# Optimization experiments

Measured on AMD Instinct MI355X. Metric: run time of the kernel, lower is better.

The kernel has to match this reference:

```python
import jax, jax.numpy as jnp
import numpy as np

V = 50304   # vocab
P = 1024    # max positions
D = 768     # model dim
H = 12      # heads
HD = D // H # head dim (64)
L = 12      # depth
M = 4       # mlp ratio
B = 2
S = 1024
LN_EPS_BLOCK = 1e-6
LN_EPS_FINAL = 1e-5


def setup_inputs() -> dict:
    key = jax.random.key(0)
    ks = jax.random.split(key, 16)
    def n(k, shape, s=0.02):
        return (jax.random.normal(k, shape) * s).astype(jnp.float32)
    inp = {
        'input_ids': jax.random.randint(ks[0], (B, S), 0, V, dtype=jnp.int64) if jax.config.jax_enable_x64 else jax.random.randint(ks[0], (B, S), 0, V).astype(jnp.int32),
        'attention_mask': jnp.ones((B, S), jnp.float32),
        'wte': n(ks[1], (V, D)),
        'wpe': n(ks[2], (P, D)),
        'ln1_g': jnp.ones((L, D), jnp.float32),
        'ln1_b': jnp.zeros((L, D), jnp.float32),
        'qkv_w': n(ks[3], (L, D, 3 * D)),
        'qkv_b': jnp.zeros((L, 3 * D), jnp.float32),
        'proj_w': n(ks[4], (L, D, D)),
        'proj_b': jnp.zeros((L, D), jnp.float32),
        'ln2_g': jnp.ones((L, D), jnp.float32),
        'ln2_b': jnp.zeros((L, D), jnp.float32),
        'fc1_w': n(ks[5], (L, D, M * D)),
        'fc1_b': jnp.zeros((L, M * D), jnp.float32),
        'fc2_w': n(ks[6], (L, M * D, D)),
        'fc2_b': jnp.zeros((L, D), jnp.float32),
        'lnf_g': jnp.ones((D,), jnp.float32),
        'lnf_b': jnp.zeros((D,), jnp.float32),
        'head_b': jnp.zeros((V,), jnp.float32),
    }
    return inp


def _ln(x, g, b, eps):
    mu = jnp.mean(x, -1, keepdims=True)
    var = jnp.mean(jnp.square(x - mu), -1, keepdims=True)
    return (x - mu) * jax.lax.rsqrt(var + eps) * g + b


def _block(x, mask_add, p):
    (g1, b1, wqkv, bqkv, wp, bp, g2, b2, w1, b1m, w2, b2m) = p
    h = _ln(x, g1, b1, LN_EPS_BLOCK)
    qkv = h @ wqkv + bqkv                                  # [B,S,3D]
    qkv = qkv.reshape(x.shape[0], x.shape[1], H, 3 * HD).transpose(0, 2, 1, 3)
    q, k, v = jnp.split(qkv, 3, axis=-1)                   # each [B,H,S,hd]
    scores = jnp.einsum('bhqd,bhkd->bhqk', q, k) / np.float32(np.sqrt(HD))
    causal = jnp.tril(jnp.ones((x.shape[1], x.shape[1]), bool))
    scores = jnp.where(causal, scores, jnp.float32(-10000.0))
    scores = scores + mask_add
    probs = jax.nn.softmax(scores, axis=-1)
    o = jnp.einsum('bhqk,bhkd->bhqd', probs, v)
    o = o.transpose(0, 2, 1, 3).reshape(x.shape[0], x.shape[1], D)
    x = x + (o @ wp + bp)
    h = _ln(x, g2, b2, LN_EPS_BLOCK)
    h = jax.nn.gelu(h @ w1 + b1m, approximate=False)
    x = x + (h @ w2 + b2m)
    return x


def reference(input_ids, attention_mask, wte, wpe, ln1_g, ln1_b, qkv_w, qkv_b,
              proj_w, proj_b, ln2_g, ln2_b, fc1_w, fc1_b, fc2_w, fc2_b,
              lnf_g, lnf_b, head_b):
    seq = input_ids.shape[1]
    mask_add = (1.0 - attention_mask)[:, None, None, :] * jnp.float32(-10000.0)
    x = wte[input_ids] + wpe[jnp.arange(seq)][None]         # [B,S,D]
    layer_params = (ln1_g, ln1_b, qkv_w, qkv_b, proj_w, proj_b,
                    ln2_g, ln2_b, fc1_w, fc1_b, fc2_w, fc2_b)
    def step(h, p):
        return _block(h, mask_add, p), None
    x, _ = jax.lax.scan(step, x, layer_params)
    x = _ln(x, lnf_g, lnf_b, LN_EPS_FINAL)
    logits = x @ wte.T + head_b                             # tied LM head
    return logits
```

## Files before the change

kernel.cpp:

```cpp
#include <hip/hip_runtime.h>
#include <hip/hip_bf16.h>

typedef unsigned short u16;
typedef short bf16x8 __attribute__((ext_vector_type(8)));
typedef float floatx4 __attribute__((ext_vector_type(4)));
typedef u16 u16x4 __attribute__((ext_vector_type(4)));

#define DEV __device__ __forceinline__

DEV u16 f2bf(float f) {
    unsigned u = __builtin_bit_cast(unsigned, f);
    u += 0x7fffu + ((u >> 16) & 1u);
    return (u16)(u >> 16);
}
DEV float bf2f(u16 h) {
    unsigned u = ((unsigned)h) << 16;
    return __builtin_bit_cast(float, u);
}

static constexpr int Dm   = 768;
static constexpr int Hn   = 12;
static constexpr int HDn  = 64;
static constexpr int Ln   = 12;
static constexpr int Vn   = 50304;
static constexpr int Sn   = 1024;
static constexpr int Bn   = 2;
static constexpr int Tn   = Bn * Sn;
static constexpr int DMLP = 4 * Dm;

#define GLOAD_LDS16(gptr, lptr)                                                        \
    __builtin_amdgcn_global_load_lds((const __attribute__((address_space(1))) void*)(gptr), \
                                     (__attribute__((address_space(3))) void*)(lptr), 16, 0, 0)

__global__ __launch_bounds__(256) void k_cvt(const float* __restrict__ s,
                                             u16* __restrict__ d, int n4) {
    int i = blockIdx.x * 256 + threadIdx.x;
    if (i >= n4) return;
    const float4 v = *(const float4*)(s + (size_t)i * 4);
    u16x4 o;
    o[0] = f2bf(v.x); o[1] = f2bf(v.y); o[2] = f2bf(v.z); o[3] = f2bf(v.w);
    *(u16x4*)(d + (size_t)i * 4) = o;
}

__global__ __launch_bounds__(256) void k_tr(const float* __restrict__ src,
                                            u16* __restrict__ dst, int R, int C) {
    __shared__ float tile[32][33];
    const int l = blockIdx.z;
    src += (size_t)l * R * C;
    dst += (size_t)l * R * C;
    const int c0 = blockIdx.x * 32, r0 = blockIdx.y * 32;
    const int tx = threadIdx.x, ty = threadIdx.y;
#pragma unroll
    for (int i = 0; i < 4; i++)
        tile[ty + i * 8][tx] = src[(size_t)(r0 + ty + i * 8) * C + c0 + tx];
    __syncthreads();
#pragma unroll
    for (int i = 0; i < 4; i++)
        dst[(size_t)(c0 + ty + i * 8) * R + r0 + tx] = f2bf(tile[tx][ty + i * 8]);
}

__global__ __launch_bounds__(256) void k_embed(const int* __restrict__ ids,
                                               const float* __restrict__ wte,
                                               const float* __restrict__ wpe,
                                               float* __restrict__ x) {
    int idx = blockIdx.x * 256 + threadIdx.x;
    int t = idx / Dm, d = idx - t * Dm;
    int s = t & (Sn - 1);
    x[idx] = wte[(size_t)ids[t] * Dm + d] + wpe[(size_t)s * Dm + d];
}

__global__ __launch_bounds__(256) void k_ln(const float* __restrict__ x,
                                            const float* __restrict__ g,
                                            const float* __restrict__ bvec,
                                            u16* __restrict__ out, float eps) {
    const int row = blockIdx.x, tid = threadIdx.x;
    const float* xr = x + (size_t)row * Dm;
    float v0 = xr[tid], v1 = xr[tid + 256], v2 = xr[tid + 512];
    float s = v0 + v1 + v2;
    float q = v0 * v0 + v1 * v1 + v2 * v2;
#pragma unroll
    for (int off = 1; off < 64; off <<= 1) {
        s += __shfl_xor(s, off, 64);
        q += __shfl_xor(q, off, 64);
    }
    __shared__ float red[8];
    const int wid = tid >> 6;
    if ((tid & 63) == 0) { red[wid] = s; red[4 + wid] = q; }
    __syncthreads();
    s = red[0] + red[1] + red[2] + red[3];
    q = red[4] + red[5] + red[6] + red[7];
    const float mu  = s * (1.0f / Dm);
    const float var = q * (1.0f / Dm) - mu * mu;
    const float rs  = rsqrtf(var + eps);
    u16* orow = out + (size_t)row * Dm;
    orow[tid]       = f2bf((v0 - mu) * rs * g[tid]       + bvec[tid]);
    orow[tid + 256] = f2bf((v1 - mu) * rs * g[tid + 256] + bvec[tid + 256]);
    orow[tid + 512] = f2bf((v2 - mu) * rs * g[tid + 512] + bvec[tid + 512]);
}

template <int MODE>
__global__ __launch_bounds__(256) void k_gemm(const u16* __restrict__ A,
                                              const u16* __restrict__ W,
                                              const float* __restrict__ bias,
                                              float* __restrict__ outF,
                                              u16* __restrict__ outB,
                                              u16* __restrict__ outQ,
                                              u16* __restrict__ outK,
                                              u16* __restrict__ outV,
                                              int M, int N, int K) {
    __shared__ u16 sA[128 * 64];
    __shared__ u16 sW[128 * 64];
    const int tid = threadIdx.x;
    const int lane = tid & 63, wid = tid >> 6;
    const int lane16 = lane & 15, quad = lane >> 4;
    const int gx = gridDim.x;
    int bid = blockIdx.y * gx + blockIdx.x;
    bid = (bid & 7) * ((gx * gridDim.y) >> 3) + (bid >> 3);
    const int m0 = (bid % gx) * 128, n0 = (bid / gx) * 128;
    const int wm = wid & 1, wn = wid >> 1;

    floatx4 acc[4][4];
#pragma unroll
    for (int i = 0; i < 4; i++)
#pragma unroll
        for (int j = 0; j < 4; j++) acc[i][j] = (floatx4){0.f, 0.f, 0.f, 0.f};

    int kbeg = 0, kend = K;
    if (MODE == 4) {
        const int Kpart = K / (int)gridDim.z;
        kbeg = blockIdx.z * Kpart;
        kend = kbeg + Kpart;
    }

    for (int kb = kbeg; kb < kend; kb += 64) {
#pragma unroll
        for (int it = 0; it < 4; ++it) {
            int p = it * 256 + tid;
            int row = p >> 3;
            int kc = (p & 7) ^ (row & 7);
            GLOAD_LDS16(A + (size_t)(m0 + row) * K + kb + kc * 8, sA + p * 8);
            GLOAD_LDS16(W + (size_t)(n0 + row) * K + kb + kc * 8, sW + p * 8);
        }
        __syncthreads();
#pragma unroll
        for (int ks = 0; ks < 2; ++ks) {
            bf16x8 af[4], wf[4];
#pragma unroll
            for (int i = 0; i < 4; i++) {
                int m = wm * 64 + i * 16 + lane16;
                int ch = (ks * 4 + quad) ^ (m & 7);
                af[i] = *(const bf16x8*)(sA + m * 64 + ch * 8);
            }
#pragma unroll
            for (int j = 0; j < 4; j++) {
                int n = wn * 64 + j * 16 + lane16;
                int ch = (ks * 4 + quad) ^ (n & 7);
                wf[j] = *(const bf16x8*)(sW + n * 64 + ch * 8);
            }
#pragma unroll
            for (int i = 0; i < 4; i++)
#pragma unroll
                for (int j = 0; j < 4; j++)
                    acc[i][j] = __builtin_amdgcn_mfma_f32_16x16x32_bf16(af[i], wf[j], acc[i][j], 0, 0, 0);
        }
        __syncthreads();
    }

#pragma unroll
    for (int i = 0; i < 4; i++) {
        int rowb = m0 + wm * 64 + i * 16 + quad * 4;
#pragma unroll
        for (int j = 0; j < 4; j++) {
            int col = n0 + wn * 64 + j * 16 + lane16;
            float bc = bias[col];
            if (MODE == 3) {
                int h = col / 192, rem = col - h * 192;
                int which = rem >> 6, d = rem & 63;
                u16* dst = (which == 0) ? outQ : (which == 1) ? outK : outV;
                float scale = (which == 0) ? 0.125f : 1.0f;
#pragma unroll
                for (int r = 0; r < 4; r++) {
                    int t = rowb + r;
                    int b = t >> 10, s = t & (Sn - 1);
                    size_t o = ((size_t)(b * Hn + h) * Sn + s) * HDn + d;
                    dst[o] = f2bf((acc[i][j][r] + bc) * scale);
                }
            } else {
#pragma unroll
                for (int r = 0; r < 4; r++) {
                    size_t off = (size_t)(rowb + r) * N + col;
                    if (MODE == 0) {
                        outF[off] = acc[i][j][r] + bc;
                    } else if (MODE == 2) {
                        float v = acc[i][j][r] + bc;
                        float gl = 0.5f * v * (1.0f + erff(v * 0.70710678118654752f));
                        outB[off] = f2bf(gl);
                    } else {
                        float v = acc[i][j][r];
                        if (blockIdx.z == 0) v += bc;
                        atomicAdd(outF + off, v);
                    }
                }
            }
        }
    }
}

__global__ __launch_bounds__(256) void k_attn(const u16* __restrict__ Q,
                                              const u16* __restrict__ Kg,
                                              const u16* __restrict__ Vg,
                                              const float* __restrict__ amask,
                                              u16* __restrict__ out) {
    __shared__ u16 sQ[64 * 72];
    __shared__ u16 sK[64 * 72];
    __shared__ u16 sV[64 * 72];
    __shared__ u16 sP[64 * 72];
    const int tid = threadIdx.x;
    const int lane = tid & 63, wid = tid >> 6;
    const int lane16 = lane & 15, quad = lane >> 4;
    const int blk = blockIdx.x;
    const int qt = blk & 15, bh = blk >> 4;
    const int b = bh / Hn, h = bh - b * Hn;
    const int q0 = qt * 64;
    const u16* Qb = Q + (size_t)bh * Sn * HDn;
    const u16* Kb = Kg + (size_t)bh * Sn * HDn;
    const u16* Vb = Vg + (size_t)bh * Sn * HDn;
    const float* maskb = amask + (size_t)b * Sn;

#pragma unroll
    for (int it = 0; it < 2; ++it) {
        int c = it * 256 + tid;
        int row = c >> 3, kc = c & 7;
        *(bf16x8*)(sQ + row * 72 + kc * 8) = *(const bf16x8*)(Qb + (size_t)(q0 + row) * HDn + kc * 8);
    }

    float mrow[4], lrow[4];
    floatx4 o[4];
#pragma unroll
    for (int r = 0; r < 4; r++) { mrow[r] = -1e30f; lrow[r] = 0.f; }
#pragma unroll
    for (int t = 0; t < 4; t++) o[t] = (floatx4){0.f, 0.f, 0.f, 0.f};

    for (int kt = 0; kt <= qt; ++kt) {
        __syncthreads();
        const int k0 = kt * 64;
#pragma unroll
        for (int it = 0; it < 2; ++it) {
            int c = it * 256 + tid;
            int row = c >> 3, kc = c & 7;
            bf16x8 kv = *(const bf16x8*)(Kb + (size_t)(k0 + row) * HDn + kc * 8);
            *(bf16x8*)(sK + row * 72 + kc * 8) = kv;
            bf16x8 vv = *(const bf16x8*)(Vb + (size_t)(k0 + row) * HDn + kc * 8);
#pragma unroll
            for (int u = 0; u < 8; u++) sV[(kc * 8 + u) * 72 + row] = (u16)vv[u];
        }
        __syncthreads();

        floatx4 s[4];
#pragma unroll
        for (int t = 0; t < 4; t++) s[t] = (floatx4){0.f, 0.f, 0.f, 0.f};
#pragma unroll
        for (int ks = 0; ks < 2; ++ks) {
            bf16x8 aq = *(const bf16x8*)(sQ + (wid * 16 + lane16) * 72 + ks * 32 + quad * 8);
#pragma unroll
            for (int t = 0; t < 4; t++) {
                bf16x8 bk = *(const bf16x8*)(sK + (t * 16 + lane16) * 72 + ks * 32 + quad * 8);
                s[t] = __builtin_amdgcn_mfma_f32_16x16x32_bf16(aq, bk, s[t], 0, 0, 0);
            }
        }

        float madd[4];
#pragma unroll
        for (int t = 0; t < 4; t++)
            madd[t] = (1.0f - maskb[k0 + t * 16 + lane16]) * -10000.0f;
#pragma unroll
        for (int t = 0; t < 4; t++) {
            int kg = k0 + t * 16 + lane16;
#pragma unroll
            for (int r = 0; r < 4; r++) {
                int qg = q0 + wid * 16 + quad * 4 + r;
                float val = s[t][r];
                if (kg > qg) val = -10000.0f;
                s[t][r] = val + madd[t];
            }
        }

        float mnew[4], alpha[4], rsum[4];
#pragma unroll
        for (int r = 0; r < 4; r++) {
            float mx = fmaxf(fmaxf(s[0][r], s[1][r]), fmaxf(s[2][r], s[3][r]));
#pragma unroll
            for (int off = 1; off < 16; off <<= 1) mx = fmaxf(mx, __shfl_xor(mx, off, 64));
            mnew[r] = fmaxf(mrow[r], mx);
            alpha[r] = expf(mrow[r] - mnew[r]);
            rsum[r] = 0.f;
        }
#pragma unroll
        for (int t = 0; t < 4; t++) {
#pragma unroll
            for (int r = 0; r < 4; r++) {
                float p = expf(s[t][r] - mnew[r]);
                rsum[r] += p;
                sP[(wid * 16 + quad * 4 + r) * 72 + t * 16 + lane16] = f2bf(p);
            }
        }
#pragma unroll
        for (int r = 0; r < 4; r++) {
#pragma unroll
            for (int off = 1; off < 16; off <<= 1) rsum[r] += __shfl_xor(rsum[r], off, 64);
            lrow[r] = lrow[r] * alpha[r] + rsum[r];
            mrow[r] = mnew[r];
        }
#pragma unroll
        for (int t = 0; t < 4; t++)
#pragma unroll
            for (int r = 0; r < 4; r++) o[t][r] *= alpha[r];

        __builtin_amdgcn_wave_barrier();

#pragma unroll
        for (int ks = 0; ks < 2; ++ks) {
            bf16x8 ap = *(const bf16x8*)(sP + (wid * 16 + lane16) * 72 + ks * 32 + quad * 8);
#pragma unroll
            for (int t = 0; t < 4; t++) {
                bf16x8 bv = *(const bf16x8*)(sV + (t * 16 + lane16) * 72 + ks * 32 + quad * 8);
                o[t] = __builtin_amdgcn_mfma_f32_16x16x32_bf16(ap, bv, o[t], 0, 0, 0);
            }
        }
    }

#pragma unroll
    for (int t = 0; t < 4; t++) {
#pragma unroll
        for (int r = 0; r < 4; r++) {
            int qg = q0 + wid * 16 + quad * 4 + r;
            float val = o[t][r] / lrow[r];
            out[(size_t)(b * Sn + qg) * Dm + h * HDn + t * 16 + lane16] = f2bf(val);
        }
    }
}

extern "C" void kernel_launch(void* const* d_in, const int* in_sizes, int n_in,
                              void* d_out, int out_size, void* d_ws, size_t ws_size,
                              hipStream_t stream) {
    (void)in_sizes; (void)n_in; (void)out_size; (void)ws_size;

    const int*   ids   = (const int*)  d_in[0];
    const float* amask = (const float*)d_in[1];
    const float* wte   = (const float*)d_in[2];
    const float* wpe   = (const float*)d_in[3];
    const float* ln1g  = (const float*)d_in[4];
    const float* ln1b  = (const float*)d_in[5];
    const float* qkvw  = (const float*)d_in[6];
    const float* qkvb  = (const float*)d_in[7];
    const float* projw = (const float*)d_in[8];
    const float* projb = (const float*)d_in[9];
    const float* ln2g  = (const float*)d_in[10];
    const float* ln2b  = (const float*)d_in[11];
    const float* fc1w  = (const float*)d_in[12];
    const float* fc1b  = (const float*)d_in[13];
    const float* fc2w  = (const float*)d_in[14];
    const float* fc2b  = (const float*)d_in[15];
    const float* lnfg  = (const float*)d_in[16];
    const float* lnfb  = (const float*)d_in[17];
    const float* headb = (const float*)d_in[18];

    char* w = (char*)d_ws;
    u16* wteB = (u16*)w;   w += (size_t)Vn * Dm * 2;
    u16* qkvW = (u16*)w;   w += (size_t)Ln * Dm * 3 * Dm * 2;
    u16* projW = (u16*)w;  w += (size_t)Ln * Dm * Dm * 2;
    u16* fc1W = (u16*)w;   w += (size_t)Ln * Dm * DMLP * 2;
    u16* fc2W = (u16*)w;   w += (size_t)Ln * DMLP * Dm * 2;
    float* x  = (float*)w; w += (size_t)Tn * Dm * 4;
    u16* hbuf = (u16*)w;   w += (size_t)Tn * Dm * 2;
    u16* qb   = (u16*)w;   w += (size_t)Tn * Dm * 2;
    u16* kb   = (u16*)w;   w += (size_t)Tn * Dm * 2;
    u16* vb   = (u16*)w;   w += (size_t)Tn * Dm * 2;
    u16* attn = (u16*)w;   w += (size_t)Tn * Dm * 2;
    u16* mlp  = (u16*)w;   w += (size_t)Tn * DMLP * 2;

    k_cvt<<<(Vn * Dm / 4) / 256, 256, 0, stream>>>(wte, wteB, Vn * Dm / 4);
    dim3 tb(32, 8);
    k_tr<<<dim3(3 * Dm / 32, Dm / 32, Ln), tb, 0, stream>>>(qkvw, qkvW, Dm, 3 * Dm);
    k_tr<<<dim3(Dm / 32, Dm / 32, Ln), tb, 0, stream>>>(projw, projW, Dm, Dm);
    k_tr<<<dim3(DMLP / 32, Dm / 32, Ln), tb, 0, stream>>>(fc1w, fc1W, Dm, DMLP);
    k_tr<<<dim3(Dm / 32, DMLP / 32, Ln), tb, 0, stream>>>(fc2w, fc2W, DMLP, Dm);

    k_embed<<<Tn * Dm / 256, 256, 0, stream>>>(ids, wte, wpe, x);

    for (int l = 0; l < Ln; ++l) {
        k_ln<<<Tn, 256, 0, stream>>>(x, ln1g + l * Dm, ln1b + l * Dm, hbuf, 1e-6f);
        k_gemm<3><<<dim3(Tn / 128, 3 * Dm / 128), 256, 0, stream>>>(
            hbuf, qkvW + (size_t)l * 3 * Dm * Dm, qkvb + l * 3 * Dm,
            nullptr, nullptr, qb, kb, vb, Tn, 3 * Dm, Dm);
        k_attn<<<Bn * Hn * (Sn / 64), 256, 0, stream>>>(qb, kb, vb, amask, attn);
        k_gemm<4><<<dim3(Tn / 128, Dm / 128, 4), 256, 0, stream>>>(
            attn, projW + (size_t)l * Dm * Dm, projb + l * Dm,
            x, nullptr, nullptr, nullptr, nullptr, Tn, Dm, Dm);
        k_ln<<<Tn, 256, 0, stream>>>(x, ln2g + l * Dm, ln2b + l * Dm, hbuf, 1e-6f);
        k_gemm<2><<<dim3(Tn / 128, DMLP / 128), 256, 0, stream>>>(
            hbuf, fc1W + (size_t)l * Dm * DMLP, fc1b + l * DMLP,
            nullptr, mlp, nullptr, nullptr, nullptr, Tn, DMLP, Dm);
        k_gemm<4><<<dim3(Tn / 128, Dm / 128, 4), 256, 0, stream>>>(
            mlp, fc2W + (size_t)l * DMLP * Dm, fc2b + l * Dm,
            x, nullptr, nullptr, nullptr, nullptr, Tn, Dm, DMLP);
    }

    k_ln<<<Tn, 256, 0, stream>>>(x, lnfg, lnfb, hbuf, 1e-5f);
    k_gemm<0><<<dim3(Tn / 128, Vn / 128), 256, 0, stream>>>(
        hbuf, wteB, headb, (float*)d_out, nullptr, nullptr, nullptr, nullptr,
        Tn, Vn, Dm);
}
```

Before: 3.209 ms.

## Add dedicated 256x128 double-buffered LM-head GEMM and raise MFMA priority in attention

```diff
diff --git a/kernel.cpp b/kernel.cpp
--- a/kernel.cpp
+++ b/kernel.cpp
@@ -206,6 +206,107 @@
     }
 }
 
+DEV void hstage(const u16* __restrict__ A, const u16* __restrict__ W, int K,
+                int m0, int n0, int kb, u16* sA, u16* sB, int tid) {
+#pragma unroll
+    for (int it = 0; it < 4; ++it) {
+        int p = it * 512 + tid;
+        int row = p >> 3;
+        int kc = (p & 7) ^ (row & 7);
+        GLOAD_LDS16(A + (size_t)(m0 + row) * K + kb + kc * 8, sA + p * 8);
+    }
+#pragma unroll
+    for (int it = 0; it < 2; ++it) {
+        int p = it * 512 + tid;
+        int row = p >> 3;
+        int kc = (p & 7) ^ (row & 7);
+        GLOAD_LDS16(W + (size_t)(n0 + row) * K + kb + kc * 8, sB + p * 8);
+    }
+}
+
+__global__ __launch_bounds__(512, 2) void k_hgemm(const u16* __restrict__ A,
+                                                  const u16* __restrict__ W,
+                                                  const float* __restrict__ bias,
+                                                  float* __restrict__ outF,
+                                                  int M, int N, int K) {
+    __shared__ u16 sA[2][256 * 64];
+    __shared__ u16 sB[2][128 * 64];
+    const int tid = threadIdx.x;
+    const int lane = tid & 63, wid = tid >> 6;
+    const int lane16 = lane & 15, quad = lane >> 4;
+    const int gxM = M >> 8;
+    int b = blockIdx.x;
+    int nb = (b & 7) * ((int)gridDim.x >> 3) + (b >> 3);
+    const int m0 = (nb % gxM) * 256;
+    const int n0 = (nb / gxM) * 128;
+    const int wm = wid & 3, wn = wid >> 2;
+
+    floatx4 acc[4][4];
+#pragma unroll
+    for (int i = 0; i < 4; i++)
+#pragma unroll
+        for (int j = 0; j < 4; j++) acc[i][j] = (floatx4){0.f, 0.f, 0.f, 0.f};
+
+    const int KT = K >> 6;
+    hstage(A, W, K, m0, n0, 0, sA[0], sB[0], tid);
+    hstage(A, W, K, m0, n0, 64, sA[1], sB[1], tid);
+
+    for (int kt = 0; kt < KT; ++kt) {
+        const int p = kt & 1;
+        if (kt + 1 < KT) asm volatile("s_waitcnt vmcnt(6)" ::: "memory");
+        else             asm volatile("s_waitcnt vmcnt(0)" ::: "memory");
+        __builtin_amdgcn_s_barrier();
+
+        bf16x8 af[2][4], wf[2][4];
+#pragma unroll
+        for (int ks = 0; ks < 2; ++ks) {
+#pragma unroll
+            for (int i = 0; i < 4; i++) {
+                int m = wm * 64 + i * 16 + lane16;
+                int ch = (ks * 4 + quad) ^ (m & 7);
+                af[ks][i] = *(const bf16x8*)(sA[p] + m * 64 + ch * 8);
+            }
+#pragma unroll
+            for (int j = 0; j < 4; j++) {
+                int n = wn * 64 + j * 16 + lane16;
+                int ch = (ks * 4 + quad) ^ (n & 7);
+                wf[ks][j] = *(const bf16x8*)(sB[p] + n * 64 + ch * 8);
+            }
+        }
+        asm volatile("s_waitcnt lgkmcnt(0)" ::: "memory");
+        __builtin_amdgcn_sched_barrier(0);
+        __builtin_amdgcn_s_barrier();
+
+        if (kt + 2 < KT)
+            hstage(A, W, K, m0, n0, (kt + 2) << 6, sA[p], sB[p], tid);
+
+        __builtin_amdgcn_s_setprio(1);
+#pragma unroll
+        for (int ks = 0; ks < 2; ++ks)
+#pragma unroll
+            for (int i = 0; i < 4; i++)
+#pragma unroll
+                for (int j = 0; j < 4; j++)
+                    acc[i][j] = __builtin_amdgcn_mfma_f32_16x16x32_bf16(af[ks][i], wf[ks][j], acc[i][j], 0, 0, 0);
+        __builtin_amdgcn_s_setprio(0);
+    }
+
+#pragma unroll
+    for (int i = 0; i < 4; i++) {
+        int rowb = m0 + wm * 64 + i * 16 + quad * 4;
+#pragma unroll
+        for (int j = 0; j < 4; j++) {
+            int col = n0 + wn * 64 + j * 16 + lane16;
+            float bc = bias[col];
+#pragma unroll
+            for (int r = 0; r < 4; r++) {
+                size_t off = (size_t)(rowb + r) * N + col;
+                outF[off] = acc[i][j][r] + bc;
+            }
+        }
+    }
+}
+
 __global__ __launch_bounds__(256) void k_attn(const u16* __restrict__ Q,
                                               const u16* __restrict__ Kg,
                                               const u16* __restrict__ Vg,
@@ -259,6 +360,7 @@
         floatx4 s[4];
 #pragma unroll
         for (int t = 0; t < 4; t++) s[t] = (floatx4){0.f, 0.f, 0.f, 0.f};
+        __builtin_amdgcn_s_setprio(1);
 #pragma unroll
         for (int ks = 0; ks < 2; ++ks) {
             bf16x8 aq = *(const bf16x8*)(sQ + (wid * 16 + lane16) * 72 + ks * 32 + quad * 8);
@@ -268,6 +370,7 @@
                 s[t] = __builtin_amdgcn_mfma_f32_16x16x32_bf16(aq, bk, s[t], 0, 0, 0);
             }
         }
+        __builtin_amdgcn_s_setprio(0);
 
         float madd[4];
 #pragma unroll
@@ -318,6 +421,7 @@
 
         __builtin_amdgcn_wave_barrier();
 
+        __builtin_amdgcn_s_setprio(1);
 #pragma unroll
         for (int ks = 0; ks < 2; ++ks) {
             bf16x8 ap = *(const bf16x8*)(sP + (wid * 16 + lane16) * 72 + ks * 32 + quad * 8);
@@ -327,6 +431,7 @@
                 o[t] = __builtin_amdgcn_mfma_f32_16x16x32_bf16(ap, bv, o[t], 0, 0, 0);
             }
         }
+        __builtin_amdgcn_s_setprio(0);
     }
 
 #pragma unroll
@@ -407,7 +512,6 @@
     }
 
     k_ln<<<Tn, 256, 0, stream>>>(x, lnfg, lnfb, hbuf, 1e-5f);
-    k_gemm<0><<<dim3(Tn / 128, Vn / 128), 256, 0, stream>>>(
-        hbuf, wteB, headb, (float*)d_out, nullptr, nullptr, nullptr, nullptr,
-        Tn, Vn, Dm);
-}
+    k_hgemm<<<(Tn / 256) * (Vn / 128), 512, 0, stream>>>(
+        hbuf, wteB, headb, (float*)d_out, Tn, Vn, Dm);
+}
```

New measurement: 3.126 ms. 2.6% less time.
